# Optimization experiments

Measured on AMD Instinct MI355X. Metric: run time of the kernel, lower is better.

Reference implementation:

```python
import jax, jax.numpy as jnp
import numpy as np

BS, X_RW, H = 16384, 768, 256  # batch, x + R*W, hidden
D_IN = X_RW + 2 * H            # 1280 = x + R*W + 2*h


def setup_inputs() -> dict:
    key = jax.random.key(0)
    ks = jax.random.split(key, 13)
    scale = 1.0 / np.sqrt(D_IN)  # nn.Linear default init range
    def lin(kw, kb):
        w = jax.random.uniform(kw, (D_IN, H), jnp.float32, -scale, scale)
        b = jax.random.uniform(kb, (H,), jnp.float32, -scale, scale)
        return w, b
    Wi, bi = lin(ks[0], ks[1])
    Wf, bf = lin(ks[2], ks[3])
    Wo, bo = lin(ks[4], ks[5])
    Ws, bs_ = lin(ks[6], ks[7])
    return {
        "input_x": jax.random.normal(ks[8], (BS, X_RW), jnp.float32),
        "previous_time": jax.random.normal(ks[9], (BS, H), jnp.float32),
        "previous_layer": jax.random.normal(ks[10], (BS, H), jnp.float32),
        "old_state": jax.random.normal(ks[11], (BS, H), jnp.float32),
        "Wi": Wi, "bi": bi, "Wf": Wf, "bf": bf,
        "Wo": Wo, "bo": bo, "Ws": Ws, "bs_": bs_,
    }


def reference(input_x, previous_time, previous_layer, old_state,
              Wi, bi, Wf, bf, Wo, bo, Ws, bs_):
    # concat once, fuse the four gate GEMMs into one [D_IN, 4H] GEMM
    s = jnp.concatenate([input_x, previous_time, previous_layer], axis=1)  # [bs, D_IN]
    W4 = jnp.concatenate([Wi, Wf, Wo, Ws], axis=1)   # [D_IN, 4H]
    b4 = jnp.concatenate([bi, bf, bo, bs_], axis=0)  # [4H]
    g = s @ W4 + b4                                   # [bs, 4H]
    i_g, f_g, o_g, c_g = jnp.split(g, 4, axis=1)
    input_gate = jax.nn.sigmoid(i_g)
    forget_gate = jax.nn.sigmoid(f_g)
    output_gate = jax.nn.sigmoid(o_g)
    new_state = forget_gate * old_state + input_gate * jnp.tanh(c_g)
    new_hidden = output_gate * jnp.tanh(new_state)
    return (new_hidden, new_state)
```

## Files before the change

kernel.cpp:

```cpp
#include <hip/hip_runtime.h>
#include <stdint.h>

#define BS   16384
#define XRW  768
#define HD   256
#define DIN  1280
#define N4   1024
#define NKT  20

typedef __attribute__((ext_vector_type(4))) float f32x4;
typedef __attribute__((ext_vector_type(8))) short s16x8;
typedef __attribute__((ext_vector_type(4))) unsigned int u32x4;

__device__ __forceinline__ unsigned short f2bf(float f) {
  uint32_t u = __builtin_bit_cast(uint32_t, f);
  u += 0x7FFFu + ((u >> 16) & 1u);
  return (unsigned short)(u >> 16);
}
__device__ __forceinline__ uint32_t cvtpk(float a, float b) {
  uint32_t d;
  asm("v_cvt_pk_bf16_f32 %0, %1, %2" : "=v"(d) : "v"(a), "v"(b));
  return d;
}
__device__ __forceinline__ float sigmoidf_(float x) {
  return 1.0f / (1.0f + __expf(-x));
}
__device__ __forceinline__ float tanhf_(float x) {
  return 1.0f - 2.0f / (__expf(2.0f * x) + 1.0f);
}
__device__ __forceinline__ void gload16(const void* g, void* l) {
  __builtin_amdgcn_global_load_lds((const __attribute__((address_space(1))) void*)g,
                                   (__attribute__((address_space(3))) void*)l, 16, 0, 0);
}

__global__ __launch_bounds__(256) void conv_w_kernel(const float* __restrict__ Wi,
                                                     const float* __restrict__ Wf,
                                                     const float* __restrict__ Wo,
                                                     const float* __restrict__ Ws,
                                                     unsigned short* __restrict__ Wt) {
  __shared__ float tile[64][65];
  const int b  = blockIdx.x;
  const int g  = b & 3;
  const int t  = b >> 2;
  const int k0 = (t % 20) * 64;
  const int h0 = (t / 20) * 64;
  const float* W = (g == 0) ? Wi : (g == 1) ? Wf : (g == 2) ? Wo : Ws;

  const int tr = threadIdx.x >> 4;
  const int tc = (threadIdx.x & 15) * 4;
  #pragma unroll
  for (int rr = 0; rr < 4; ++rr) {
    const int r = rr * 16 + tr;
    f32x4 v = *(const f32x4*)(W + (size_t)(k0 + r) * HD + h0 + tc);
    tile[r][tc + 0] = v.x; tile[r][tc + 1] = v.y;
    tile[r][tc + 2] = v.z; tile[r][tc + 3] = v.w;
  }
  __syncthreads();

  const int hl = threadIdx.x >> 2;
  const int kc = (threadIdx.x & 3) * 16;
  const int h  = h0 + hl;
  const int np = (h >> 4) * 64 + g * 16 + (h & 15);
  s16x8 o0, o1;
  #pragma unroll
  for (int j = 0; j < 8; ++j) {
    o0[j] = (short)f2bf(tile[kc + j][hl]);
    o1[j] = (short)f2bf(tile[kc + 8 + j][hl]);
  }
  *(s16x8*)(Wt + (size_t)np * DIN + k0 + kc)     = o0;
  *(s16x8*)(Wt + (size_t)np * DIN + k0 + kc + 8) = o1;
}

__global__ __launch_bounds__(512, 2)
void lstm_gemm_kernel(const float* __restrict__ X,
                      const float* __restrict__ PT,
                      const float* __restrict__ PL,
                      const unsigned short* __restrict__ Wt,
                      const float* __restrict__ BI,
                      const float* __restrict__ BF,
                      const float* __restrict__ BO,
                      const float* __restrict__ BSv,
                      const float* __restrict__ OLD,
                      float* __restrict__ out) {
  __shared__ unsigned char smem[131072];
  const int tid  = threadIdx.x;
  const int wid  = tid >> 6;
  const int lane = tid & 63;

  const int H = blockIdx.x;
  const int xcd = H & 7, slot = H >> 3;
  const int mt = xcd * 8 + (slot >> 2);
  const int nt = slot & 3;
  const int wr = wid >> 2, wc = wid & 3;

  const int r8   = lane >> 3;
  const int scol = ((lane & 7) ^ r8) << 4;
  const char* gB = (const char*)Wt + (size_t)(nt * 256 + wid * 8 + r8) * (DIN * 2) + scol;

#define STAGE_B(t1, oB) do {                                                  \
    const int kb_ = (t1) * 128;                                               \
    _Pragma("unroll")                                                         \
    for (int c_ = 0; c_ < 4; ++c_)                                            \
      gload16(gB + (size_t)c_ * (64 * DIN * 2) + kb_,                         \
              &smem[65536 + (oB) + c_ * 8192 + wid * 1024]);                  \
  } while (0)

  const int arow  = tid >> 3;
  const int a7    = tid & 7;
  const int awcol = ((a7 ^ (arow & 7)) << 4);

#define ALOAD(t1, h, R0, R1, R2, R3) do {                                     \
    const float* asrc_; int astr_, aoff_;                                     \
    if ((t1) < 12)      { asrc_ = X;  astr_ = XRW; aoff_ = (t1) * 64; }       \
    else if ((t1) < 16) { asrc_ = PT; astr_ = HD;  aoff_ = ((t1) - 12) * 64; }\
    else                { asrc_ = PL; astr_ = HD;  aoff_ = ((t1) - 16) * 64; }\
    const float* ga_ = asrc_ + (size_t)(mt * 256 + arow + (h) * 128) * astr_  \
                             + aoff_ + a7 * 8;                                \
    R0 = *(const f32x4*)(ga_);                                                \
    R1 = *(const f32x4*)(ga_ + 4);                                            \
    R2 = *(const f32x4*)(ga_ + (size_t)64 * astr_);                           \
    R3 = *(const f32x4*)(ga_ + (size_t)64 * astr_ + 4);                       \
  } while (0)

#define AWRITE(oB, h, R0, R1, R2, R3) do {                                    \
    u32x4 w0_, w1_;                                                           \
    w0_.x = cvtpk(R0.x, R0.y); w0_.y = cvtpk(R0.z, R0.w);                     \
    w0_.z = cvtpk(R1.x, R1.y); w0_.w = cvtpk(R1.z, R1.w);                     \
    w1_.x = cvtpk(R2.x, R2.y); w1_.y = cvtpk(R2.z, R2.w);                     \
    w1_.z = cvtpk(R3.x, R3.y); w1_.w = cvtpk(R3.z, R3.w);                     \
    *(u32x4*)(&smem[(oB) + ((arow + (h) * 128)      << 7) + awcol]) = w0_;    \
    *(u32x4*)(&smem[(oB) + ((arow + (h) * 128 + 64) << 7) + awcol]) = w1_;    \
  } while (0)

  const int rx   = lane & 15;
  const int axor = (lane & 7) << 4;
  const int col0 = (((lane >> 4) << 4)) ^ axor;
  const int col1 = (64 + ((lane >> 4) << 4)) ^ axor;
  const int aRow = (wr * 128 + rx) * 128;
  const int bRow = 65536 + (wc * 64 + rx) * 128;

  f32x4 acc[8][4];
  #pragma unroll
  for (int i = 0; i < 8; ++i)
    #pragma unroll
    for (int j = 0; j < 4; ++j) {
      f32x4 z = {0.0f, 0.0f, 0.0f, 0.0f};
      acc[i][j] = z;
    }

#define VMW(N) asm volatile("s_waitcnt vmcnt(" #N ")" ::: "memory")
#define LGKM0() do { asm volatile("s_waitcnt lgkmcnt(0)" ::: "memory");       \
                     __builtin_amdgcn_sched_barrier(0); } while (0)
#define FRAGS(bo_, kh_col) do {                                               \
    _Pragma("unroll")                                                         \
    for (int nf = 0; nf < 4; ++nf)                                            \
      bq[nf] = *(const s16x8*)(&smem[(bo_) + bRow + nf * 2048 + (kh_col)]);   \
    _Pragma("unroll")                                                         \
    for (int mf = 0; mf < 8; ++mf)                                            \
      aq[mf] = *(const s16x8*)(&smem[(bo_) + aRow + mf * 2048 + (kh_col)]);   \
  } while (0)
#define MFMAS() do {                                                          \
    __builtin_amdgcn_s_setprio(1);                                            \
    _Pragma("unroll")                                                         \
    for (int mf = 0; mf < 8; ++mf)                                            \
      _Pragma("unroll")                                                       \
      for (int nf = 0; nf < 4; ++nf)                                          \
        acc[mf][nf] = __builtin_amdgcn_mfma_f32_16x16x32_bf16(aq[mf], bq[nf], \
                                                      acc[mf][nf], 0, 0, 0);  \
    __builtin_amdgcn_s_setprio(0);                                            \
  } while (0)

  {
    f32x4 p0, p1, p2, p3;
    ALOAD(0, 0, p0, p1, p2, p3);
    STAGE_B(0, 0);
    VMW(4);
    AWRITE(0, 0, p0, p1, p2, p3);
    ALOAD(0, 1, p0, p1, p2, p3);
    VMW(0);
    AWRITE(0, 1, p0, p1, p2, p3);
    LGKM0();
    __builtin_amdgcn_s_barrier();
  }

  for (int kt = 0; kt < NKT; ++kt) {
    const int c = kt & 1, o = c ^ 1;
    const int bo_ = c << 15;
    const int oo_ = o << 15;
    const bool pf = (kt + 1) < NKT;
    s16x8 aq[8], bq[4];
    f32x4 ar0, ar1, ar2, ar3;

    if (pf) ALOAD(kt + 1, 0, ar0, ar1, ar2, ar3);
    FRAGS(bo_, col0);
    if (pf) STAGE_B(kt + 1, oo_);
    MFMAS();
    VMW(4);
    if (pf) { AWRITE(oo_, 0, ar0, ar1, ar2, ar3); ALOAD(kt + 1, 1, ar0, ar1, ar2, ar3); }
    FRAGS(bo_, col1);
    MFMAS();
    VMW(0);
    if (pf) AWRITE(oo_, 1, ar0, ar1, ar2, ar3);
    LGKM0();
    __builtin_amdgcn_s_barrier();
  }

  {
    const int hq = nt * 64 + wc * 16 + rx;
    const float bbi = BI[hq], bbf = BF[hq], bbo = BO[hq], bbs = BSv[hq];
    const int m0 = mt * 256 + wr * 128 + (lane >> 4) * 4;
    float* outNS = out + (size_t)BS * HD;
    float oldc[4], oldn[4];
    #pragma unroll
    for (int r = 0; r < 4; ++r)
      oldc[r] = OLD[(size_t)(m0 + r) * HD + hq];
    #pragma unroll
    for (int mf = 0; mf < 8; ++mf) {
      const int mrow = m0 + mf * 16;
      if (mf < 7) {
        #pragma unroll
        for (int r = 0; r < 4; ++r)
          oldn[r] = OLD[(size_t)(mrow + 16 + r) * HD + hq];
      }
      #pragma unroll
      for (int r = 0; r < 4; ++r) {
        const float ig = sigmoidf_(acc[mf][0][r] + bbi);
        const float fg = sigmoidf_(acc[mf][1][r] + bbf);
        const float og = sigmoidf_(acc[mf][2][r] + bbo);
        const float cg = tanhf_(acc[mf][3][r] + bbs);
        const float ns = fg * oldc[r] + ig * cg;
        const float nh = og * tanhf_(ns);
        __builtin_nontemporal_store(nh, &out[(size_t)(mrow + r) * HD + hq]);
        __builtin_nontemporal_store(ns, &outNS[(size_t)(mrow + r) * HD + hq]);
      }
      #pragma unroll
      for (int r = 0; r < 4; ++r)
        oldc[r] = oldn[r];
    }
  }
#undef STAGE_B
#undef ALOAD
#undef AWRITE
#undef VMW
#undef LGKM0
#undef FRAGS
#undef MFMAS
}

extern "C" void kernel_launch(void* const* d_in, const int* in_sizes, int n_in,
                              void* d_out, int out_size, void* d_ws, size_t ws_size,
                              hipStream_t stream) {
  const float* X   = (const float*)d_in[0];
  const float* PT  = (const float*)d_in[1];
  const float* PL  = (const float*)d_in[2];
  const float* OLD = (const float*)d_in[3];
  const float* Wi  = (const float*)d_in[4];
  const float* bi  = (const float*)d_in[5];
  const float* Wf  = (const float*)d_in[6];
  const float* bfv = (const float*)d_in[7];
  const float* Wo  = (const float*)d_in[8];
  const float* bo  = (const float*)d_in[9];
  const float* Ws  = (const float*)d_in[10];
  const float* bsv = (const float*)d_in[11];
  float* out = (float*)d_out;

  unsigned short* Wt = (unsigned short*)d_ws;

  conv_w_kernel<<<320, 256, 0, stream>>>(Wi, Wf, Wo, Ws, Wt);
  lstm_gemm_kernel<<<256, 512, 0, stream>>>(X, PT, PL, Wt, bi, bfv, bo, bsv, OLD, out);
}
```

Before: 58.17 us.

## Shrink GEMM block tile to 256x128 with K-step 32 and 4 waves

The LSTM gate GEMM now uses a 256x128 output tile per block with a K-step of 32 instead of a 256x256 tile with a K-step of 64. The block drops from 8 waves to 4 and LDS from 128KB to 48KB, and 512 blocks are launched instead of 256. Swizzle patterns and index maps are rewritten to match. The aim is to use more of the CUs and allow several blocks per CU. In exchange, each A tile is loaded twice as often across blocks, and the loop runs twice as many barrier-synchronised iterations, each with less MFMA work.

```diff
diff --git a/kernel.cpp b/kernel.cpp
--- a/kernel.cpp
+++ b/kernel.cpp
@@ -6,7 +6,7 @@
 #define HD   256
 #define DIN  1280
 #define N4   1024
-#define NKT  20
+#define NKT  40
 
 typedef __attribute__((ext_vector_type(4))) float f32x4;
 typedef __attribute__((ext_vector_type(8))) short s16x8;
@@ -71,7 +71,7 @@
   *(s16x8*)(Wt + (size_t)np * DIN + k0 + kc + 8) = o1;
 }
 
-__global__ __launch_bounds__(512, 2)
+__global__ __launch_bounds__(256, 2)
 void lstm_gemm_kernel(const float* __restrict__ X,
                       const float* __restrict__ PT,
                       const float* __restrict__ PL,
@@ -82,62 +82,62 @@
                       const float* __restrict__ BSv,
                       const float* __restrict__ OLD,
                       float* __restrict__ out) {
-  __shared__ unsigned char smem[131072];
+  __shared__ unsigned char smem[49152];
   const int tid  = threadIdx.x;
   const int wid  = tid >> 6;
   const int lane = tid & 63;
 
   const int H = blockIdx.x;
   const int xcd = H & 7, slot = H >> 3;
-  const int mt = xcd * 8 + (slot >> 2);
-  const int nt = slot & 3;
-  const int wr = wid >> 2, wc = wid & 3;
-
-  const int r8   = lane >> 3;
-  const int scol = ((lane & 7) ^ r8) << 4;
-  const char* gB = (const char*)Wt + (size_t)(nt * 256 + wid * 8 + r8) * (DIN * 2) + scol;
+  const int mt = xcd * 8 + (slot >> 3);
+  const int nt = slot & 7;
+  const int wr = wid >> 1, wc = wid & 1;
+
+  const int bscol = ((tid & 3) ^ ((tid >> 3) & 3)) << 4;
+  const char* gB = (const char*)Wt + (size_t)(nt * 128 + (tid >> 2)) * (DIN * 2) + bscol;
 
 #define STAGE_B(t1, oB) do {                                                  \
-    const int kb_ = (t1) * 128;                                               \
-    _Pragma("unroll")                                                         \
-    for (int c_ = 0; c_ < 4; ++c_)                                            \
-      gload16(gB + (size_t)c_ * (64 * DIN * 2) + kb_,                         \
-              &smem[65536 + (oB) + c_ * 8192 + wid * 1024]);                  \
-  } while (0)
-
-  const int arow  = tid >> 3;
-  const int a7    = tid & 7;
-  const int awcol = ((a7 ^ (arow & 7)) << 4);
+    _Pragma("unroll")                                                         \
+    for (int c_ = 0; c_ < 2; ++c_)                                            \
+      gload16(gB + (size_t)c_ * (64 * DIN * 2) + (t1) * 64,                   \
+              &smem[32768 + (oB) + c_ * 4096 + tid * 16]);                    \
+  } while (0)
+
+  const int arow_ = tid >> 1;
+  const int ak    = (tid & 1) * 16;
+  const int as_   = (tid >> 2) & 3;
+  const int au0   = (tid & 1) * 2;
+  const int aw0   = (au0 ^ as_) << 4;
+  const int aw1   = ((au0 + 1) ^ as_) << 4;
 
 #define ALOAD(t1, h, R0, R1, R2, R3) do {                                     \
     const float* asrc_; int astr_, aoff_;                                     \
-    if ((t1) < 12)      { asrc_ = X;  astr_ = XRW; aoff_ = (t1) * 64; }       \
-    else if ((t1) < 16) { asrc_ = PT; astr_ = HD;  aoff_ = ((t1) - 12) * 64; }\
-    else                { asrc_ = PL; astr_ = HD;  aoff_ = ((t1) - 16) * 64; }\
-    const float* ga_ = asrc_ + (size_t)(mt * 256 + arow + (h) * 128) * astr_  \
-                             + aoff_ + a7 * 8;                                \
+    if ((t1) < 24)      { asrc_ = X;  astr_ = XRW; aoff_ = (t1) * 32; }       \
+    else if ((t1) < 32) { asrc_ = PT; astr_ = HD;  aoff_ = ((t1) - 24) * 32; }\
+    else                { asrc_ = PL; astr_ = HD;  aoff_ = ((t1) - 32) * 32; }\
+    const float* ga_ = asrc_ + (size_t)(mt * 256 + arow_ + (h) * 128) * astr_ \
+                             + aoff_ + ak;                                    \
     R0 = *(const f32x4*)(ga_);                                                \
     R1 = *(const f32x4*)(ga_ + 4);                                            \
-    R2 = *(const f32x4*)(ga_ + (size_t)64 * astr_);                           \
-    R3 = *(const f32x4*)(ga_ + (size_t)64 * astr_ + 4);                       \
-  } while (0)
-
-#define AWRITE(oB, h, R0, R1, R2, R3) do {                                    \
-    u32x4 w0_, w1_;                                                           \
-    w0_.x = cvtpk(R0.x, R0.y); w0_.y = cvtpk(R0.z, R0.w);                     \
-    w0_.z = cvtpk(R1.x, R1.y); w0_.w = cvtpk(R1.z, R1.w);                     \
-    w1_.x = cvtpk(R2.x, R2.y); w1_.y = cvtpk(R2.z, R2.w);                     \
-    w1_.z = cvtpk(R3.x, R3.y); w1_.w = cvtpk(R3.z, R3.w);                     \
-    *(u32x4*)(&smem[(oB) + ((arow + (h) * 128)      << 7) + awcol]) = w0_;    \
-    *(u32x4*)(&smem[(oB) + ((arow + (h) * 128 + 64) << 7) + awcol]) = w1_;    \
+    R2 = *(const f32x4*)(ga_ + 8);                                            \
+    R3 = *(const f32x4*)(ga_ + 12);                                           \
+  } while (0)
+
+#define AWRITE(oA, h, R0, R1, R2, R3) do {                                    \
+    u32x4 wlo_, whi_;                                                         \
+    wlo_.x = cvtpk(R0.x, R0.y); wlo_.y = cvtpk(R0.z, R0.w);                   \
+    wlo_.z = cvtpk(R1.x, R1.y); wlo_.w = cvtpk(R1.z, R1.w);                   \
+    whi_.x = cvtpk(R2.x, R2.y); whi_.y = cvtpk(R2.z, R2.w);                   \
+    whi_.z = cvtpk(R3.x, R3.y); whi_.w = cvtpk(R3.z, R3.w);                   \
+    const int rb_ = (oA) + ((arow_ + (h) * 128) << 6);                        \
+    *(u32x4*)(&smem[rb_ + aw0]) = wlo_;                                       \
+    *(u32x4*)(&smem[rb_ + aw1]) = whi_;                                       \
   } while (0)
 
   const int rx   = lane & 15;
-  const int axor = (lane & 7) << 4;
-  const int col0 = (((lane >> 4) << 4)) ^ axor;
-  const int col1 = (64 + ((lane >> 4) << 4)) ^ axor;
-  const int aRow = (wr * 128 + rx) * 128;
-  const int bRow = 65536 + (wc * 64 + rx) * 128;
+  const int colq = ((lane >> 4) ^ ((rx >> 1) & 3)) << 4;
+  const int aRow = (wr * 128 + rx) * 64;
+  const int bRow = 32768 + (wc * 64 + rx) * 64;
 
   f32x4 acc[8][4];
   #pragma unroll
@@ -151,18 +151,18 @@
 #define VMW(N) asm volatile("s_waitcnt vmcnt(" #N ")" ::: "memory")
 #define LGKM0() do { asm volatile("s_waitcnt lgkmcnt(0)" ::: "memory");       \
                      __builtin_amdgcn_sched_barrier(0); } while (0)
-#define FRAGS(bo_, kh_col) do {                                               \
+#define FRAGS(aB, bB) do {                                                    \
     _Pragma("unroll")                                                         \
     for (int nf = 0; nf < 4; ++nf)                                            \
-      bq[nf] = *(const s16x8*)(&smem[(bo_) + bRow + nf * 2048 + (kh_col)]);   \
+      bq[nf] = *(const s16x8*)(&smem[(bB) + bRow + nf * 1024 + colq]);        \
     _Pragma("unroll")                                                         \
     for (int mf = 0; mf < 8; ++mf)                                            \
-      aq[mf] = *(const s16x8*)(&smem[(bo_) + aRow + mf * 2048 + (kh_col)]);   \
-  } while (0)
-#define MFMAS() do {                                                          \
+      aq[mf] = *(const s16x8*)(&smem[(aB) + aRow + mf * 1024 + colq]);        \
+  } while (0)
+#define MFH(m0_) do {                                                         \
     __builtin_amdgcn_s_setprio(1);                                            \
     _Pragma("unroll")                                                         \
-    for (int mf = 0; mf < 8; ++mf)                                            \
+    for (int mf = (m0_); mf < (m0_) + 4; ++mf)                                \
       _Pragma("unroll")                                                       \
       for (int nf = 0; nf < 4; ++nf)                                          \
         acc[mf][nf] = __builtin_amdgcn_mfma_f32_16x16x32_bf16(aq[mf], bq[nf], \
@@ -174,7 +174,7 @@
     f32x4 p0, p1, p2, p3;
     ALOAD(0, 0, p0, p1, p2, p3);
     STAGE_B(0, 0);
-    VMW(4);
+    VMW(2);
     AWRITE(0, 0, p0, p1, p2, p3);
     ALOAD(0, 1, p0, p1, p2, p3);
     VMW(0);
@@ -184,29 +184,27 @@
   }
 
   for (int kt = 0; kt < NKT; ++kt) {
-    const int c = kt & 1, o = c ^ 1;
-    const int bo_ = c << 15;
-    const int oo_ = o << 15;
+    const int aB = (kt & 1) << 14, aO = aB ^ 16384;
+    const int bB = (kt & 1) << 13, bO = bB ^ 8192;
     const bool pf = (kt + 1) < NKT;
     s16x8 aq[8], bq[4];
     f32x4 ar0, ar1, ar2, ar3;
 
     if (pf) ALOAD(kt + 1, 0, ar0, ar1, ar2, ar3);
-    FRAGS(bo_, col0);
-    if (pf) STAGE_B(kt + 1, oo_);
-    MFMAS();
-    VMW(4);
-    if (pf) { AWRITE(oo_, 0, ar0, ar1, ar2, ar3); ALOAD(kt + 1, 1, ar0, ar1, ar2, ar3); }
-    FRAGS(bo_, col1);
-    MFMAS();
+    FRAGS(aB, bB);
+    if (pf) STAGE_B(kt + 1, bO);
+    MFH(0);
+    VMW(2);
+    if (pf) { AWRITE(aO, 0, ar0, ar1, ar2, ar3); ALOAD(kt + 1, 1, ar0, ar1, ar2, ar3); }
+    MFH(4);
     VMW(0);
-    if (pf) AWRITE(oo_, 1, ar0, ar1, ar2, ar3);
+    if (pf) AWRITE(aO, 1, ar0, ar1, ar2, ar3);
     LGKM0();
     __builtin_amdgcn_s_barrier();
   }
 
   {
-    const int hq = nt * 64 + wc * 16 + rx;
+    const int hq = (nt * 2 + wc) * 16 + rx;
     const float bbi = BI[hq], bbf = BF[hq], bbo = BO[hq], bbs = BSv[hq];
     const int m0 = mt * 256 + wr * 128 + (lane >> 4) * 4;
     float* outNS = out + (size_t)BS * HD;
@@ -244,7 +242,7 @@
 #undef VMW
 #undef LGKM0
 #undef FRAGS
-#undef MFMAS
+#undef MFH
 }
 
 extern "C" void kernel_launch(void* const* d_in, const int* in_sizes, int n_in,
@@ -267,5 +265,5 @@
   unsigned short* Wt = (unsigned short*)d_ws;
 
   conv_w_kernel<<<320, 256, 0, stream>>>(Wi, Wf, Wo, Ws, Wt);
-  lstm_gemm_kernel<<<256, 512, 0, stream>>>(X, PT, PL, Wt, bi, bfv, bo, bsv, OLD, out);
-}
+  lstm_gemm_kernel<<<512, 256, 0, stream>>>(X, PT, PL, Wt, bi, bfv, bo, bsv, OLD, out);
+}
```

New measurement: 81.99 us. 40.9% more time.

## Triple-buffer weight tiles in LDS and prefetch them two K-steps ahead

Applied to the files above, without the earlier changes.

B (weight) tiles get a three-slot LDS ring, and each step issues the async global-to-LDS load for tile t+2 rather than t+1. The A buffer stays double-buffered, and the main loop is unrolled by six to keep buffer indices static. The explicit vmcnt waits are removed, so ordering now relies on the compiler-inserted waits for the A register loads. LDS use grows to 160KB, which removes headroom, and the async loads may now be under-synchronized.

```diff
diff --git a/kernel.cpp b/kernel.cpp
--- a/kernel.cpp
+++ b/kernel.cpp
@@ -82,7 +82,7 @@
                       const float* __restrict__ BSv,
                       const float* __restrict__ OLD,
                       float* __restrict__ out) {
-  __shared__ unsigned char smem[131072];
+  __shared__ unsigned char smem[163840];
   const int tid  = threadIdx.x;
   const int wid  = tid >> 6;
   const int lane = tid & 63;
@@ -97,12 +97,12 @@
   const int scol = ((lane & 7) ^ r8) << 4;
   const char* gB = (const char*)Wt + (size_t)(nt * 256 + wid * 8 + r8) * (DIN * 2) + scol;
 
-#define STAGE_B(t1, oB) do {                                                  \
+#define STAGE_B(t1, bb) do {                                                  \
     const int kb_ = (t1) * 128;                                               \
     _Pragma("unroll")                                                         \
     for (int c_ = 0; c_ < 4; ++c_)                                            \
       gload16(gB + (size_t)c_ * (64 * DIN * 2) + kb_,                         \
-              &smem[65536 + (oB) + c_ * 8192 + wid * 1024]);                  \
+              &smem[65536 + (bb) * 32768 + c_ * 8192 + wid * 1024]);          \
   } while (0)
 
   const int arow  = tid >> 3;
@@ -122,14 +122,14 @@
     R3 = *(const f32x4*)(ga_ + (size_t)64 * astr_ + 4);                       \
   } while (0)
 
-#define AWRITE(oB, h, R0, R1, R2, R3) do {                                    \
+#define AWRITE(ab, h, R0, R1, R2, R3) do {                                    \
     u32x4 w0_, w1_;                                                           \
     w0_.x = cvtpk(R0.x, R0.y); w0_.y = cvtpk(R0.z, R0.w);                     \
     w0_.z = cvtpk(R1.x, R1.y); w0_.w = cvtpk(R1.z, R1.w);                     \
     w1_.x = cvtpk(R2.x, R2.y); w1_.y = cvtpk(R2.z, R2.w);                     \
     w1_.z = cvtpk(R3.x, R3.y); w1_.w = cvtpk(R3.z, R3.w);                     \
-    *(u32x4*)(&smem[(oB) + ((arow + (h) * 128)      << 7) + awcol]) = w0_;    \
-    *(u32x4*)(&smem[(oB) + ((arow + (h) * 128 + 64) << 7) + awcol]) = w1_;    \
+    *(u32x4*)(&smem[(ab) * 32768 + ((arow + (h) * 128)      << 7) + awcol]) = w0_; \
+    *(u32x4*)(&smem[(ab) * 32768 + ((arow + (h) * 128 + 64) << 7) + awcol]) = w1_; \
   } while (0)
 
   const int rx   = lane & 15;
@@ -137,7 +137,7 @@
   const int col0 = (((lane >> 4) << 4)) ^ axor;
   const int col1 = (64 + ((lane >> 4) << 4)) ^ axor;
   const int aRow = (wr * 128 + rx) * 128;
-  const int bRow = 65536 + (wc * 64 + rx) * 128;
+  const int bRow = (wc * 64 + rx) * 128;
 
   f32x4 acc[8][4];
   #pragma unroll
@@ -148,16 +148,15 @@
       acc[i][j] = z;
     }
 
-#define VMW(N) asm volatile("s_waitcnt vmcnt(" #N ")" ::: "memory")
 #define LGKM0() do { asm volatile("s_waitcnt lgkmcnt(0)" ::: "memory");       \
                      __builtin_amdgcn_sched_barrier(0); } while (0)
-#define FRAGS(bo_, kh_col) do {                                               \
+#define FRAGS(ab, bb, kh_col) do {                                            \
     _Pragma("unroll")                                                         \
     for (int nf = 0; nf < 4; ++nf)                                            \
-      bq[nf] = *(const s16x8*)(&smem[(bo_) + bRow + nf * 2048 + (kh_col)]);   \
+      bq[nf] = *(const s16x8*)(&smem[65536 + (bb) * 32768 + bRow + nf * 2048 + (kh_col)]); \
     _Pragma("unroll")                                                         \
     for (int mf = 0; mf < 8; ++mf)                                            \
-      aq[mf] = *(const s16x8*)(&smem[(bo_) + aRow + mf * 2048 + (kh_col)]);   \
+      aq[mf] = *(const s16x8*)(&smem[(ab) * 32768 + aRow + mf * 2048 + (kh_col)]); \
   } while (0)
 #define MFMAS() do {                                                          \
     __builtin_amdgcn_s_setprio(1);                                            \
@@ -170,40 +169,44 @@
     __builtin_amdgcn_s_setprio(0);                                            \
   } while (0)
 
+#define TILE(t1, AB, BR, BW, PFA, PFB) do {                                   \
+    s16x8 aq[8], bq[4];                                                       \
+    f32x4 ar0, ar1, ar2, ar3;                                                 \
+    if (PFA) ALOAD((t1) + 1, 0, ar0, ar1, ar2, ar3);                          \
+    FRAGS(AB, BR, col0);                                                      \
+    MFMAS();                                                                  \
+    if (PFA) { AWRITE((AB) ^ 1, 0, ar0, ar1, ar2, ar3);                       \
+               ALOAD((t1) + 1, 1, ar0, ar1, ar2, ar3); }                      \
+    FRAGS(AB, BR, col1);                                                      \
+    MFMAS();                                                                  \
+    if (PFA) AWRITE((AB) ^ 1, 1, ar0, ar1, ar2, ar3);                         \
+    if (PFB) STAGE_B((t1) + 2, BW);                                           \
+    LGKM0();                                                                  \
+    __builtin_amdgcn_s_barrier();                                             \
+  } while (0)
+
   {
     f32x4 p0, p1, p2, p3;
     ALOAD(0, 0, p0, p1, p2, p3);
     STAGE_B(0, 0);
-    VMW(4);
+    STAGE_B(1, 1);
     AWRITE(0, 0, p0, p1, p2, p3);
     ALOAD(0, 1, p0, p1, p2, p3);
-    VMW(0);
     AWRITE(0, 1, p0, p1, p2, p3);
     LGKM0();
     __builtin_amdgcn_s_barrier();
   }
 
-  for (int kt = 0; kt < NKT; ++kt) {
-    const int c = kt & 1, o = c ^ 1;
-    const int bo_ = c << 15;
-    const int oo_ = o << 15;
-    const bool pf = (kt + 1) < NKT;
-    s16x8 aq[8], bq[4];
-    f32x4 ar0, ar1, ar2, ar3;
-
-    if (pf) ALOAD(kt + 1, 0, ar0, ar1, ar2, ar3);
-    FRAGS(bo_, col0);
-    if (pf) STAGE_B(kt + 1, oo_);
-    MFMAS();
-    VMW(4);
-    if (pf) { AWRITE(oo_, 0, ar0, ar1, ar2, ar3); ALOAD(kt + 1, 1, ar0, ar1, ar2, ar3); }
-    FRAGS(bo_, col1);
-    MFMAS();
-    VMW(0);
-    if (pf) AWRITE(oo_, 1, ar0, ar1, ar2, ar3);
-    LGKM0();
-    __builtin_amdgcn_s_barrier();
-  }
+  for (int j = 0; j < 18; j += 6) {
+    TILE(j + 0, 0, 0, 2, true, true);
+    TILE(j + 1, 1, 1, 0, true, true);
+    TILE(j + 2, 0, 2, 1, true, true);
+    TILE(j + 3, 1, 0, 2, true, true);
+    TILE(j + 4, 0, 1, 0, true, true);
+    TILE(j + 5, 1, 2, 1, true, true);
+  }
+  TILE(18, 0, 0, 2, true, false);
+  TILE(19, 1, 1, 0, false, false);
 
   {
     const int hq = nt * 64 + wc * 16 + rx;
@@ -241,10 +244,10 @@
 #undef STAGE_B
 #undef ALOAD
 #undef AWRITE
-#undef VMW
 #undef LGKM0
 #undef FRAGS
 #undef MFMAS
+#undef TILE
 }
 
 extern "C" void kernel_launch(void* const* d_in, const int* in_sizes, int n_in,
```

Result: slower. 90.77 us (+56.0%).

## Use 4 waves per block with 128x128 warp tiles instead of 8 waves

Applied to the files above, without the earlier changes.

The GEMM block drops from 512 to 256 threads. Each wave now computes a 128x128 output tile (8x8 MFMA fragments) instead of 128x64, so fragment reuse per LDS read goes up. The A and B staging loops and the epilogue are rewritten so each thread loads more data and handles two hidden columns. This trades latency hiding from having more waves for better register-level reuse, and risks register pressure from 256 accumulator VGPRs per thread.

```diff
diff --git a/kernel.cpp b/kernel.cpp
--- a/kernel.cpp
+++ b/kernel.cpp
@@ -71,7 +71,7 @@
   *(s16x8*)(Wt + (size_t)np * DIN + k0 + kc + 8) = o1;
 }
 
-__global__ __launch_bounds__(512, 2)
+__global__ __launch_bounds__(256, 1)
 void lstm_gemm_kernel(const float* __restrict__ X,
                       const float* __restrict__ PT,
                       const float* __restrict__ PL,
@@ -91,45 +91,48 @@
   const int xcd = H & 7, slot = H >> 3;
   const int mt = xcd * 8 + (slot >> 2);
   const int nt = slot & 3;
-  const int wr = wid >> 2, wc = wid & 3;
-
-  const int r8   = lane >> 3;
-  const int scol = ((lane & 7) ^ r8) << 4;
-  const char* gB = (const char*)Wt + (size_t)(nt * 256 + wid * 8 + r8) * (DIN * 2) + scol;
+  const int wr = wid >> 1, wc = wid & 1;
+
+  const int r5   = tid >> 3;
+  const int scol = ((tid & 7) ^ (r5 & 7)) << 4;
+  const char* gB = (const char*)Wt + (size_t)(nt * 256 + r5) * (DIN * 2) + scol;
 
 #define STAGE_B(t1, oB) do {                                                  \
     const int kb_ = (t1) * 128;                                               \
     _Pragma("unroll")                                                         \
-    for (int c_ = 0; c_ < 4; ++c_)                                            \
-      gload16(gB + (size_t)c_ * (64 * DIN * 2) + kb_,                         \
-              &smem[65536 + (oB) + c_ * 8192 + wid * 1024]);                  \
-  } while (0)
-
-  const int arow  = tid >> 3;
-  const int a7    = tid & 7;
-  const int awcol = ((a7 ^ (arow & 7)) << 4);
-
-#define ALOAD(t1, h, R0, R1, R2, R3) do {                                     \
+    for (int c_ = 0; c_ < 8; ++c_)                                            \
+      gload16(gB + (size_t)c_ * (32 * DIN * 2) + kb_,                         \
+              &smem[65536 + (oB) + c_ * 4096 + tid * 16]);                    \
+  } while (0)
+
+  const int arow4 = tid >> 2;
+  const int ak4   = (tid & 3) * 16;
+  const int as4   = arow4 & 7;
+  const int aw0   = (((tid & 3) * 2)     ^ as4) << 4;
+  const int aw1   = (((tid & 3) * 2 + 1) ^ as4) << 4;
+
+#define ALOAD(t1, q, R0, R1, R2, R3) do {                                     \
     const float* asrc_; int astr_, aoff_;                                     \
     if ((t1) < 12)      { asrc_ = X;  astr_ = XRW; aoff_ = (t1) * 64; }       \
     else if ((t1) < 16) { asrc_ = PT; astr_ = HD;  aoff_ = ((t1) - 12) * 64; }\
     else                { asrc_ = PL; astr_ = HD;  aoff_ = ((t1) - 16) * 64; }\
-    const float* ga_ = asrc_ + (size_t)(mt * 256 + arow + (h) * 128) * astr_  \
-                             + aoff_ + a7 * 8;                                \
+    const float* ga_ = asrc_ + (size_t)(mt * 256 + (q) * 64 + arow4) * astr_  \
+                             + aoff_ + ak4;                                   \
     R0 = *(const f32x4*)(ga_);                                                \
     R1 = *(const f32x4*)(ga_ + 4);                                            \
-    R2 = *(const f32x4*)(ga_ + (size_t)64 * astr_);                           \
-    R3 = *(const f32x4*)(ga_ + (size_t)64 * astr_ + 4);                       \
-  } while (0)
-
-#define AWRITE(oB, h, R0, R1, R2, R3) do {                                    \
+    R2 = *(const f32x4*)(ga_ + 8);                                            \
+    R3 = *(const f32x4*)(ga_ + 12);                                           \
+  } while (0)
+
+#define AWRITE(ab, q, R0, R1, R2, R3) do {                                    \
     u32x4 w0_, w1_;                                                           \
     w0_.x = cvtpk(R0.x, R0.y); w0_.y = cvtpk(R0.z, R0.w);                     \
     w0_.z = cvtpk(R1.x, R1.y); w0_.w = cvtpk(R1.z, R1.w);                     \
     w1_.x = cvtpk(R2.x, R2.y); w1_.y = cvtpk(R2.z, R2.w);                     \
     w1_.z = cvtpk(R3.x, R3.y); w1_.w = cvtpk(R3.z, R3.w);                     \
-    *(u32x4*)(&smem[(oB) + ((arow + (h) * 128)      << 7) + awcol]) = w0_;    \
-    *(u32x4*)(&smem[(oB) + ((arow + (h) * 128 + 64) << 7) + awcol]) = w1_;    \
+    const int rb_ = (ab) + (((q) * 64 + arow4) << 7);                         \
+    *(u32x4*)(&smem[rb_ + aw0]) = w0_;                                        \
+    *(u32x4*)(&smem[rb_ + aw1]) = w1_;                                        \
   } while (0)
 
   const int rx   = lane & 15;
@@ -137,13 +140,13 @@
   const int col0 = (((lane >> 4) << 4)) ^ axor;
   const int col1 = (64 + ((lane >> 4) << 4)) ^ axor;
   const int aRow = (wr * 128 + rx) * 128;
-  const int bRow = 65536 + (wc * 64 + rx) * 128;
-
-  f32x4 acc[8][4];
+  const int bRow = 65536 + (wc * 128 + rx) * 128;
+
+  f32x4 acc[8][8];
   #pragma unroll
   for (int i = 0; i < 8; ++i)
     #pragma unroll
-    for (int j = 0; j < 4; ++j) {
+    for (int j = 0; j < 8; ++j) {
       f32x4 z = {0.0f, 0.0f, 0.0f, 0.0f};
       acc[i][j] = z;
     }
@@ -153,7 +156,7 @@
                      __builtin_amdgcn_sched_barrier(0); } while (0)
 #define FRAGS(bo_, kh_col) do {                                               \
     _Pragma("unroll")                                                         \
-    for (int nf = 0; nf < 4; ++nf)                                            \
+    for (int nf = 0; nf < 8; ++nf)                                            \
       bq[nf] = *(const s16x8*)(&smem[(bo_) + bRow + nf * 2048 + (kh_col)]);   \
     _Pragma("unroll")                                                         \
     for (int mf = 0; mf < 8; ++mf)                                            \
@@ -164,21 +167,25 @@
     _Pragma("unroll")                                                         \
     for (int mf = 0; mf < 8; ++mf)                                            \
       _Pragma("unroll")                                                       \
-      for (int nf = 0; nf < 4; ++nf)                                          \
+      for (int nf = 0; nf < 8; ++nf)                                          \
         acc[mf][nf] = __builtin_amdgcn_mfma_f32_16x16x32_bf16(aq[mf], bq[nf], \
                                                       acc[mf][nf], 0, 0, 0);  \
     __builtin_amdgcn_s_setprio(0);                                            \
   } while (0)
 
   {
-    f32x4 p0, p1, p2, p3;
+    f32x4 p0, p1, p2, p3, q0, q1, q2, q3;
     ALOAD(0, 0, p0, p1, p2, p3);
+    ALOAD(0, 1, q0, q1, q2, q3);
     STAGE_B(0, 0);
-    VMW(4);
+    VMW(8);
     AWRITE(0, 0, p0, p1, p2, p3);
-    ALOAD(0, 1, p0, p1, p2, p3);
+    AWRITE(0, 1, q0, q1, q2, q3);
+    ALOAD(0, 2, p0, p1, p2, p3);
+    ALOAD(0, 3, q0, q1, q2, q3);
     VMW(0);
-    AWRITE(0, 1, p0, p1, p2, p3);
+    AWRITE(0, 2, p0, p1, p2, p3);
+    AWRITE(0, 3, q0, q1, q2, q3);
     LGKM0();
     __builtin_amdgcn_s_barrier();
   }
@@ -188,54 +195,76 @@
     const int bo_ = c << 15;
     const int oo_ = o << 15;
     const bool pf = (kt + 1) < NKT;
-    s16x8 aq[8], bq[4];
-    f32x4 ar0, ar1, ar2, ar3;
-
-    if (pf) ALOAD(kt + 1, 0, ar0, ar1, ar2, ar3);
+    s16x8 aq[8], bq[8];
+    f32x4 p0, p1, p2, p3, q0, q1, q2, q3;
+
+    if (pf) { ALOAD(kt + 1, 0, p0, p1, p2, p3);
+              ALOAD(kt + 1, 1, q0, q1, q2, q3); }
     FRAGS(bo_, col0);
     if (pf) STAGE_B(kt + 1, oo_);
     MFMAS();
-    VMW(4);
-    if (pf) { AWRITE(oo_, 0, ar0, ar1, ar2, ar3); ALOAD(kt + 1, 1, ar0, ar1, ar2, ar3); }
+    VMW(8);
+    if (pf) { AWRITE(oo_, 0, p0, p1, p2, p3);
+              AWRITE(oo_, 1, q0, q1, q2, q3);
+              ALOAD(kt + 1, 2, p0, p1, p2, p3);
+              ALOAD(kt + 1, 3, q0, q1, q2, q3); }
     FRAGS(bo_, col1);
     MFMAS();
     VMW(0);
-    if (pf) AWRITE(oo_, 1, ar0, ar1, ar2, ar3);
+    if (pf) { AWRITE(oo_, 2, p0, p1, p2, p3);
+              AWRITE(oo_, 3, q0, q1, q2, q3); }
     LGKM0();
     __builtin_amdgcn_s_barrier();
   }
 
   {
-    const int hq = nt * 64 + wc * 16 + rx;
-    const float bbi = BI[hq], bbf = BF[hq], bbo = BO[hq], bbs = BSv[hq];
+    const int hq0 = (nt * 4 + wc * 2) * 16 + rx;
+    const int hq1 = hq0 + 16;
+    const float bi0 = BI[hq0], bf0 = BF[hq0], bo0 = BO[hq0], bs0 = BSv[hq0];
+    const float bi1 = BI[hq1], bf1 = BF[hq1], bo1 = BO[hq1], bs1 = BSv[hq1];
     const int m0 = mt * 256 + wr * 128 + (lane >> 4) * 4;
     float* outNS = out + (size_t)BS * HD;
-    float oldc[4], oldn[4];
+    float oc0[4], oc1[4], on0[4], on1[4];
     #pragma unroll
-    for (int r = 0; r < 4; ++r)
-      oldc[r] = OLD[(size_t)(m0 + r) * HD + hq];
+    for (int r = 0; r < 4; ++r) {
+      oc0[r] = OLD[(size_t)(m0 + r) * HD + hq0];
+      oc1[r] = OLD[(size_t)(m0 + r) * HD + hq1];
+    }
     #pragma unroll
     for (int mf = 0; mf < 8; ++mf) {
       const int mrow = m0 + mf * 16;
       if (mf < 7) {
         #pragma unroll
-        for (int r = 0; r < 4; ++r)
-          oldn[r] = OLD[(size_t)(mrow + 16 + r) * HD + hq];
+        for (int r = 0; r < 4; ++r) {
+          on0[r] = OLD[(size_t)(mrow + 16 + r) * HD + hq0];
+          on1[r] = OLD[(size_t)(mrow + 16 + r) * HD + hq1];
+        }
       }
       #pragma unroll
       for (int r = 0; r < 4; ++r) {
-        const float ig = sigmoidf_(acc[mf][0][r] + bbi);
-        const float fg = sigmoidf_(acc[mf][1][r] + bbf);
-        const float og = sigmoidf_(acc[mf][2][r] + bbo);
-        const float cg = tanhf_(acc[mf][3][r] + bbs);
-        const float ns = fg * oldc[r] + ig * cg;
-        const float nh = og * tanhf_(ns);
-        __builtin_nontemporal_store(nh, &out[(size_t)(mrow + r) * HD + hq]);
-        __builtin_nontemporal_store(ns, &outNS[(size_t)(mrow + r) * HD + hq]);
+        {
+          const float ig = sigmoidf_(acc[mf][0][r] + bi0);
+          const float fg = sigmoidf_(acc[mf][1][r] + bf0);
+          const float og = sigmoidf_(acc[mf][2][r] + bo0);
+          const float cg = tanhf_(acc[mf][3][r] + bs0);
+          const float ns = fg * oc0[r] + ig * cg;
+          const float nh = og * tanhf_(ns);
+          __builtin_nontemporal_store(nh, &out[(size_t)(mrow + r) * HD + hq0]);
+          __builtin_nontemporal_store(ns, &outNS[(size_t)(mrow + r) * HD + hq0]);
+        }
+        {
+          const float ig = sigmoidf_(acc[mf][4][r] + bi1);
+          const float fg = sigmoidf_(acc[mf][5][r] + bf1);
+          const float og = sigmoidf_(acc[mf][6][r] + bo1);
+          const float cg = tanhf_(acc[mf][7][r] + bs1);
+          const float ns = fg * oc1[r] + ig * cg;
+          const float nh = og * tanhf_(ns);
+          __builtin_nontemporal_store(nh, &out[(size_t)(mrow + r) * HD + hq1]);
+          __builtin_nontemporal_store(ns, &outNS[(size_t)(mrow + r) * HD + hq1]);
+        }
       }
       #pragma unroll
-      for (int r = 0; r < 4; ++r)
-        oldc[r] = oldn[r];
+      for (int r = 0; r < 4; ++r) { oc0[r] = on0[r]; oc1[r] = on1[r]; }
     }
   }
 #undef STAGE_B
@@ -267,5 +296,5 @@
   unsigned short* Wt = (unsigned short*)d_ws;
 
   conv_w_kernel<<<320, 256, 0, stream>>>(Wi, Wf, Wo, Ws, Wt);
-  lstm_gemm_kernel<<<256, 512, 0, stream>>>(X, PT, PL, Wt, bi, bfv, bo, bsv, OLD, out);
-}
+  lstm_gemm_kernel<<<256, 256, 0, stream>>>(X, PT, PL, Wt, bi, bfv, bo, bsv, OLD, out);
+}
```

New measurement: 66.64 us. 1.15x slower.
